# Performance work log

Hardware: AMD Instinct MI355X
Metric: run time of the kernel (lower is better)

## Reference

```python
import jax, jax.numpy as jnp
import numpy as np

EPS = 1e-5
H = 12  # num_heads

def ste_sign(x):
    # forward: sign(x) in {-1,+1}; backward: grad passes where |x|<1 (clip STE)
    c = jnp.clip(x, -1.0, 1.0)
    s = jnp.where(x >= 0, 1.0, -1.0).astype(x.dtype)
    return c + jax.lax.stop_gradient(s - c)

def bin_w(w):
    # adaptive per-output-channel scaling: alpha = mean|w| (detached), weight = alpha*sign(w)
    alpha = jax.lax.stop_gradient(jnp.mean(jnp.abs(w), axis=1, keepdims=True))
    return alpha * ste_sign(w)

def layernorm(x, g, b):
    mu = jnp.mean(x, axis=-1, keepdims=True)
    var = jnp.var(x, axis=-1, keepdims=True)
    return (x - mu) * jax.lax.rsqrt(var + EPS) * g + b

def setup_inputs():
    key = jax.random.key(0)
    ks = jax.random.split(key, 6)
    B, N, C, hid = 8, 1024, 768, 3072
    s = 0.02
    return {
        "x": jax.random.normal(ks[0], (B, N, C), jnp.float32),
        "ln1_g": jnp.ones((C,), jnp.float32),
        "ln1_b": jnp.zeros((C,), jnp.float32),
        "w_qkv": jax.random.normal(ks[1], (3 * C, C), jnp.float32) * s,
        "w_proj": jax.random.normal(ks[2], (C, C), jnp.float32) * s,
        "b_proj": jnp.zeros((C,), jnp.float32),
        "ls1_g": 1e-5 * jnp.ones((C,), jnp.float32),
        "ln2_g": jnp.ones((C,), jnp.float32),
        "ln2_b": jnp.zeros((C,), jnp.float32),
        "w_fc1": jax.random.normal(ks[3], (hid, C), jnp.float32) * s,
        "b_fc1": jnp.zeros((hid,), jnp.float32),
        "w_fc2": jax.random.normal(ks[4], (C, hid), jnp.float32) * s,
        "b_fc2": jnp.zeros((C,), jnp.float32),
        "ls2_g": 1e-5 * jnp.ones((C,), jnp.float32),
    }

def reference(x, ln1_g, ln1_b, w_qkv, w_proj, b_proj, ls1_g, ln2_g, ln2_b, w_fc1, b_fc1, w_fc2, b_fc2, ls2_g):
    B, N, C = x.shape
    hd = C // H
    scale = hd ** -0.5
    # --- binarized attention ---
    h = layernorm(x, ln1_g, ln1_b)
    qkv = jnp.einsum('bnc,oc->bno', ste_sign(h), bin_w(w_qkv))        # 1w1a qkv proj
    qkv = qkv.reshape(B, N, 3, H, hd).transpose(2, 0, 3, 1, 4)        # [3,B,H,N,hd]
    bqkv = ste_sign(qkv)                                              # BinaryQuantizer
    q, k, v = bqkv[0], bqkv[1], bqkv[2]
    attn = jnp.einsum('bhnd,bhmd->bhnm', q, k) * scale                # [B,H,N,N]
    sm = jax.nn.softmax(attn, axis=-1)
    abin = (attn > 0).astype(x.dtype)                                 # SoftmaxBinaryQuantizer fwd value
    attn_eff = sm + jax.lax.stop_gradient(abin - sm)                  # STE: fwd=binary, bwd=softmax
    o = jnp.einsum('bhnm,bhmd->bhnd', attn_eff, v)
    o = o.transpose(0, 2, 1, 3).reshape(B, N, C)
    o = jnp.einsum('bnc,oc->bno', ste_sign(o), bin_w(w_proj)) + b_proj
    x = x + ls1_g * o
    # --- binary MLP (1-bit weight, 32-bit activation) ---
    h2 = layernorm(x, ln2_g, ln2_b)
    m = jax.nn.gelu(jnp.einsum('bnc,hc->bnh', h2, bin_w(w_fc1)) + b_fc1, approximate=False)
    m = jnp.einsum('bnh,ch->bnc', m, bin_w(w_fc2)) + b_fc2
    return x + ls2_g * m
```

## Files before the change

### kernel.cpp

```cpp
#include <hip/hip_runtime.h>

#define NTOK 8192
#define CDIM 768
#define HIDD 3072
#define NQKV 2304
#define SEQL 1024
#define NHEAD 12

typedef int i32x4 __attribute__((ext_vector_type(4)));
typedef float f32x4 __attribute__((ext_vector_type(4)));
typedef signed char sc16 __attribute__((ext_vector_type(16)));

__device__ __forceinline__ void gload_lds16(const void* g, void* l) {
    __builtin_amdgcn_global_load_lds(
        (const __attribute__((address_space(1))) unsigned int*)g,
        (__attribute__((address_space(3))) unsigned int*)l, 16, 0, 0);
}

__global__ void sign_w_kernel(const float* __restrict__ w, signed char* __restrict__ ws, int n) {
    int i = blockIdx.x * blockDim.x + threadIdx.x;
    int stride = gridDim.x * blockDim.x;
    for (; i < n; i += stride)
        ws[i] = (w[i] >= 0.0f) ? 1 : -1;
}

template<bool PERM>
__global__ void __launch_bounds__(256) signalpha_kernel(const float* __restrict__ w,
                                                        signed char* __restrict__ ws,
                                                        float* __restrict__ alpha, int K) {
    int row = blockIdx.x;
    const float* wr = w + (size_t)row * K;
    signed char* wsr = ws + (size_t)row * K;
    float s = 0.f;
    for (int i = threadIdx.x; i < K; i += 256) {
        float v = wr[i];
        int ip = PERM ? ((i & ~63) | (((i & 15) << 2) | ((i >> 4) & 3))) : i;
        wsr[ip] = (v >= 0.f) ? 1 : -1;
        s += fabsf(v);
    }
    for (int off = 32; off > 0; off >>= 1) s += __shfl_down(s, off);
    __shared__ float red[4];
    if ((threadIdx.x & 63) == 0) red[threadIdx.x >> 6] = s;
    __syncthreads();
    if (threadIdx.x == 0) alpha[row] = (red[0] + red[1] + red[2] + red[3]) / (float)K;
}

__global__ void __launch_bounds__(256) ln_sign_kernel(const float* __restrict__ x, const float* __restrict__ g,
                                                      const float* __restrict__ b, signed char* __restrict__ out) {
    int row = blockIdx.x;
    const float* xr = x + (size_t)row * CDIM;
    float v0 = xr[threadIdx.x], v1 = xr[threadIdx.x + 256], v2 = xr[threadIdx.x + 512];
    float s = v0 + v1 + v2, s2 = v0 * v0 + v1 * v1 + v2 * v2;
    for (int off = 32; off > 0; off >>= 1) { s += __shfl_down(s, off); s2 += __shfl_down(s2, off); }
    __shared__ float red[8];
    if ((threadIdx.x & 63) == 0) { red[threadIdx.x >> 6] = s; red[4 + (threadIdx.x >> 6)] = s2; }
    __syncthreads();
    float ts = red[0] + red[1] + red[2] + red[3];
    float t2 = red[4] + red[5] + red[6] + red[7];
    float mu = ts * (1.0f / CDIM);
    float var = t2 * (1.0f / CDIM) - mu * mu;
    float rstd = rsqrtf(var + 1e-5f);
    signed char* orow = out + (size_t)row * CDIM;
    float vv[3] = {v0, v1, v2};
#pragma unroll
    for (int p = 0; p < 3; p++) {
        int i = threadIdx.x + p * 256;
        float val = (vv[p] - mu) * rstd * g[i] + b[i];
        orow[i] = (val >= 0.f) ? 1 : -1;
    }
}

__global__ void __launch_bounds__(256) ln2q_kernel(const float* __restrict__ x, const float* __restrict__ g,
                                                   const float* __restrict__ b, signed char* __restrict__ out,
                                                   float* __restrict__ rowscale) {
    int row = blockIdx.x;
    const float* xr = x + (size_t)row * CDIM;
    float v0 = xr[threadIdx.x], v1 = xr[threadIdx.x + 256], v2 = xr[threadIdx.x + 512];
    float s = v0 + v1 + v2, s2 = v0 * v0 + v1 * v1 + v2 * v2;
    for (int off = 32; off > 0; off >>= 1) { s += __shfl_down(s, off); s2 += __shfl_down(s2, off); }
    __shared__ float red[8];
    __shared__ float redm[4];
    if ((threadIdx.x & 63) == 0) { red[threadIdx.x >> 6] = s; red[4 + (threadIdx.x >> 6)] = s2; }
    __syncthreads();
    float ts = red[0] + red[1] + red[2] + red[3];
    float t2 = red[4] + red[5] + red[6] + red[7];
    float mu = ts * (1.0f / CDIM);
    float var = t2 * (1.0f / CDIM) - mu * mu;
    float rstd = rsqrtf(var + 1e-5f);
    float a0 = (v0 - mu) * rstd * g[threadIdx.x] + b[threadIdx.x];
    float a1 = (v1 - mu) * rstd * g[threadIdx.x + 256] + b[threadIdx.x + 256];
    float a2v = (v2 - mu) * rstd * g[threadIdx.x + 512] + b[threadIdx.x + 512];
    float mx = fmaxf(fabsf(a0), fmaxf(fabsf(a1), fabsf(a2v)));
    for (int off = 32; off > 0; off >>= 1) mx = fmaxf(mx, __shfl_down(mx, off));
    if ((threadIdx.x & 63) == 0) redm[threadIdx.x >> 6] = mx;
    __syncthreads();
    float rmax = fmaxf(fmaxf(redm[0], redm[1]), fmaxf(redm[2], redm[3]));
    rmax = fmaxf(rmax, 1e-20f);
    float inv = 127.f / rmax;
    signed char* orow = out + (size_t)row * CDIM;
    orow[threadIdx.x]       = (signed char)__float2int_rn(a0 * inv);
    orow[threadIdx.x + 256] = (signed char)__float2int_rn(a1 * inv);
    orow[threadIdx.x + 512] = (signed char)__float2int_rn(a2v * inv);
    if (threadIdx.x == 0) rowscale[row] = rmax * (1.f / 127.f);
}

enum { EPI_RESID = 1, EPI_GELU = 2, EPI_QKV = 3 };
#define MSCALE_INV 16.0f

template<int EPI, int BN>
__global__ void __launch_bounds__(256) gemm_i8(
    const signed char* __restrict__ A, const signed char* __restrict__ B,
    int M, int N, int K,
    const float* __restrict__ alpha, const float* __restrict__ bias,
    const float* __restrict__ ls, const float* __restrict__ resid,
    const float* __restrict__ rowscale, float ascale,
    float* __restrict__ outF, signed char* __restrict__ outB,
    signed char* __restrict__ vtB)
{
    constexpr int STAGE_B = 3 * (128 + BN) * 64;
    static_assert(STAGE_B >= 128 * 68 * 4 || EPI != EPI_RESID, "epi lds fits");
    __shared__ __align__(16) char lds_raw[STAGE_B];
    auto As = (signed char (*)[128][64])lds_raw;
    auto Bs = (signed char (*)[BN][64])(lds_raw + 3 * 128 * 64);

    const int tid = threadIdx.x, ln = tid & 63, w = tid >> 6;
    const int wm = w >> 1, wn = w & 1;
    const int lq = ln & 15, khi = ln >> 4;
    constexpr int NF = BN / 32;
    constexpr int L = (BN == 128) ? 4 : 3;

    const int nwg = gridDim.x * gridDim.y;
    const int id = blockIdx.y * gridDim.x + blockIdx.x;
    const int nid = (id & 7) * (nwg >> 3) + (id >> 3);
    const int bxs = nid % gridDim.x, bys = nid / gridDim.x;
    const int bm = bys * 128, bn = bxs * BN;

    const i32x4 iz = {0, 0, 0, 0};
    i32x4 acc[4][NF];
#pragma unroll
    for (int m = 0; m < 4; m++)
#pragma unroll
        for (int n = 0; n < NF; n++) acc[m][n] = iz;

    const int srow = tid >> 2, scol = (tid & 3) * 16;
    const int ssrc = ((tid & 3) ^ ((srow >> 1) & 3)) * 16;
    const int sa = 16 * (khi ^ ((lq >> 1) & 3));

    auto STAGE = [&](int p, int k0) {
        gload_lds16(A + (size_t)(bm + srow) * K + k0 + ssrc, &As[p][srow][scol]);
        gload_lds16(A + (size_t)(bm + 64 + srow) * K + k0 + ssrc, &As[p][64 + srow][scol]);
        gload_lds16(B + (size_t)(bn + srow) * K + k0 + ssrc, &Bs[p][srow][scol]);
        if constexpr (BN == 128)
            gload_lds16(B + (size_t)(bn + 64 + srow) * K + k0 + ssrc, &Bs[p][64 + srow][scol]);
    };
    auto COMPUTE = [&](int p, bool prefetch, int knext) {
        i32x4 aF[4], bF[NF];
#pragma unroll
        for (int m = 0; m < 4; m++) aF[m] = *(const i32x4*)&As[p][wm * 64 + m * 16 + lq][sa];
#pragma unroll
        for (int n = 0; n < NF; n++) bF[n] = *(const i32x4*)&Bs[p][wn * (BN / 2) + n * 16 + lq][sa];
        if (prefetch) STAGE((p + 2) % 3, knext);
        __builtin_amdgcn_s_setprio(1);
#pragma unroll
        for (int m = 0; m < 4; m++)
#pragma unroll
            for (int n = 0; n < NF; n++)
                acc[m][n] = __builtin_amdgcn_mfma_i32_16x16x64_i8(aF[m], bF[n], acc[m][n], 0, 0, 0);
        __builtin_amdgcn_s_setprio(0);
    };

    const int nst = K >> 6;
    STAGE(0, 0);
    STAGE(1, 64);
#pragma unroll 1
    for (int t = 0; t < nst - 1; t++) {
        asm volatile("s_waitcnt vmcnt(%0)" :: "n"(L) : "memory");
        __builtin_amdgcn_s_barrier();
        COMPUTE(t % 3, t + 2 < nst, (t + 2) << 6);
    }
    asm volatile("s_waitcnt vmcnt(0)" ::: "memory");
    __builtin_amdgcn_s_barrier();
    COMPUTE((nst - 1) % 3, false, 0);

    const int r0 = bm + wm * 64, c0loc = wn * (BN / 2);

    if constexpr (EPI == EPI_RESID) {
        __syncthreads();
        float (*Cf)[68] = (float (*)[68])lds_raw;
#pragma unroll
        for (int m = 0; m < 4; m++)
#pragma unroll
            for (int n = 0; n < NF; n++)
#pragma unroll
                for (int i = 0; i < 4; i++)
                    Cf[wm * 64 + m * 16 + khi * 4 + i][c0loc + n * 16 + lq] =
                        (float)acc[m][n][i] * ascale;
        __syncthreads();
#pragma unroll
        for (int p = 0; p < 8; p++) {
            int idx = p * 256 + tid;
            int row = idx >> 4, c4 = (idx & 15) * 4;
            f32x4 a4 = *(const f32x4*)&alpha[bn + c4];
            f32x4 b4 = *(const f32x4*)&bias[bn + c4];
            f32x4 l4 = *(const f32x4*)&ls[bn + c4];
            f32x4 v4 = *(const f32x4*)&Cf[row][c4];
            size_t g = (size_t)(bm + row) * N + bn + c4;
            f32x4 r4 = *(const f32x4*)&resid[g];
            f32x4 o4 = r4 + l4 * (a4 * v4 + b4);
            *(f32x4*)&outF[g] = o4;
        }
    } else if constexpr (EPI == EPI_GELU) {
        float al[NF], bi[NF];
#pragma unroll
        for (int n = 0; n < NF; n++) {
            int c = bn + c0loc + n * 16 + lq;
            al[n] = alpha[c]; bi[n] = bias[c];
        }
#pragma unroll
        for (int m = 0; m < 4; m++)
#pragma unroll
            for (int i = 0; i < 4; i++) {
                int r = r0 + m * 16 + khi * 4 + i;
                float rs = rowscale[r];
                unsigned pk = 0;
#pragma unroll
                for (int n = 0; n < NF; n++) {
                    float t = al[n] * ((float)acc[m][n][i] * rs) + bi[n];
                    float y2 = 1.5957691f * t + 0.07135481f * t * t * t;
                    float ge = t * __builtin_amdgcn_rcpf(1.0f + __expf(-y2));
                    float qf = fminf(fmaxf(ge * MSCALE_INV, -127.f), 127.f);
                    pk |= (unsigned)(unsigned char)(signed char)__float2int_rn(qf) << (8 * n);
                }
                *(unsigned*)(outB + (size_t)r * N + bn + c0loc + lq * 4) = pk;
            }
    } else {
        if (bn < 1536) {
#pragma unroll
            for (int m = 0; m < 4; m++)
#pragma unroll
                for (int i = 0; i < 4; i++) {
                    int r = r0 + m * 16 + khi * 4 + i;
                    unsigned pk = 0;
#pragma unroll
                    for (int n = 0; n < NF; n++)
                        pk |= (unsigned)(unsigned char)(signed char)((acc[m][n][i] >= 0) ? 1 : -1) << (8 * n);
                    *(unsigned*)(outB + (size_t)r * 1536 + bn + c0loc + lq * 4) = pk;
                }
        } else {
#pragma unroll
            for (int m = 0; m < 4; m++)
#pragma unroll
                for (int n = 0; n < NF; n++) {
                    int cg = bn + c0loc + n * 16 + lq - 1536;
                    int hh = cg >> 6, dd = cg & 63;
                    int rb = r0 + m * 16 + khi * 4;
                    unsigned pk = 0;
#pragma unroll
                    for (int i = 0; i < 4; i++)
                        pk |= (unsigned)(unsigned char)(signed char)((acc[m][n][i] >= 0) ? 1 : -1) << (8 * i);
                    *(unsigned*)(vtB + (((size_t)(rb >> 10) * NHEAD + hh) * 64 + dd) * SEQL + (rb & 1023)) = pk;
                }
        }
    }
}

__global__ void __launch_bounds__(256) attn_v2(const signed char* __restrict__ qk,
                                               const signed char* __restrict__ vt,
                                               signed char* __restrict__ a2) {
    const int id = blockIdx.x;
    const int nid = (id & 7) * 96 + (id >> 3);
    const int bh = nid >> 3, qb = nid & 7;
    const int b = bh / NHEAD, h = bh % NHEAD;
    const int tid = threadIdx.x, ln = tid & 63, w = tid >> 6;
    const int lq = ln & 15, khi = ln >> 4;

    __shared__ signed char Ks[64][80];
    __shared__ signed char Vts[64][80];
    __shared__ signed char Pw[4][32][80];

    const size_t tokbase = (size_t)b * SEQL;
    const int q0 = qb * 128 + w * 32;
    const int str = tid >> 2, stc = (tid & 3) * 16;
    const size_t vtrow = ((size_t)bh * 64 + str) * SEQL;

    i32x4 qfrag[2];
#pragma unroll
    for (int qf = 0; qf < 2; qf++)
        qfrag[qf] = *(const i32x4*)(qk + (tokbase + q0 + qf * 16 + lq) * 1536 + h * 64 + khi * 16);

    const i32x4 iz = {0, 0, 0, 0};
    i32x4 o[2][4];
#pragma unroll
    for (int qf = 0; qf < 2; qf++)
#pragma unroll
        for (int df = 0; df < 4; df++) o[qf][df] = iz;

    auto LOADJ = [&](int j, sc16& kr, sc16& vr) {
        kr = *(const sc16*)(qk + (tokbase + j * 64 + str) * 1536 + 768 + h * 64 + stc);
        vr = *(const sc16*)(vt + vtrow + j * 64 + stc);
    };
    auto STORE = [&](const sc16& kr, const sc16& vr) {
        *(sc16*)&Ks[str][stc] = kr;
        *(sc16*)&Vts[str][stc] = vr;
    };
    auto COMPUTE = [&]() {
        i32x4 kfrag[4];
#pragma unroll
        for (int kf = 0; kf < 4; kf++)
            kfrag[kf] = *(const i32x4*)&Ks[kf * 16 + lq][khi * 16];
#pragma unroll
        for (int kf = 0; kf < 4; kf++) {
#pragma unroll
            for (int qf = 0; qf < 2; qf++) {
                i32x4 st = __builtin_amdgcn_mfma_i32_16x16x64_i8(kfrag[kf], qfrag[qf], iz, 0, 0, 0);
                unsigned pb = (st[0] > 0 ? 1u : 0u) | (st[1] > 0 ? 0x100u : 0u) |
                              (st[2] > 0 ? 0x10000u : 0u) | (st[3] > 0 ? 0x1000000u : 0u);
                *(unsigned*)&Pw[w][qf * 16 + lq][kf * 16 + khi * 4] = pb;
            }
        }
        i32x4 pa[2];
#pragma unroll
        for (int qf = 0; qf < 2; qf++)
            pa[qf] = *(const i32x4*)&Pw[w][qf * 16 + lq][khi * 16];
#pragma unroll
        for (int df = 0; df < 4; df++) {
            i32x4 vfr = *(const i32x4*)&Vts[df * 16 + lq][khi * 16];
#pragma unroll
            for (int qf = 0; qf < 2; qf++)
                o[qf][df] = __builtin_amdgcn_mfma_i32_16x16x64_i8(pa[qf], vfr, o[qf][df], 0, 0, 0);
        }
    };

    sc16 ka, va, kb, vb;
    LOADJ(0, ka, va);
#pragma unroll 1
    for (int jj = 0; jj < 16; jj += 2) {
        __syncthreads();
        STORE(ka, va);
        __syncthreads();
        LOADJ(jj + 1, kb, vb);
        COMPUTE();
        __syncthreads();
        STORE(kb, vb);
        __syncthreads();
        if (jj + 2 < 16) LOADJ(jj + 2, ka, va);
        COMPUTE();
    }

#pragma unroll
    for (int qf = 0; qf < 2; qf++)
#pragma unroll
        for (int i = 0; i < 4; i++) {
            int qrow = q0 + qf * 16 + khi * 4 + i;
            unsigned pk = 0;
#pragma unroll
            for (int df = 0; df < 4; df++)
                pk |= (unsigned)(unsigned char)(signed char)((o[qf][df][i] >= 0) ? 1 : -1) << (8 * df);
            *(unsigned*)(a2 + (tokbase + qrow) * CDIM + h * 64 + lq * 4) = pk;
        }
}

static const size_t OFF_WQKV  = 0;
static const size_t OFF_WPROJ = 1769472;
static const size_t OFF_WFC1  = 2359296;
static const size_t OFF_WFC2  = 4718592;
static const size_t OFF_APROJ = 7077888;
static const size_t OFF_AFC1  = 7080960;
static const size_t OFF_AFC2  = 7093248;
static const size_t OFF_H2SC  = 7096320;
static const size_t OFF_QK    = 7129088;
static const size_t OFF_VT    = 19712000;
static const size_t OFF_A2    = 26003456;
static const size_t OFF_A1    = 32294912;
static const size_t OFF_M1    = 38586368;
static const size_t OFF_H2    = 63752192;

extern "C" void kernel_launch(void* const* d_in, const int* in_sizes, int n_in,
                              void* d_out, int out_size, void* d_ws, size_t ws_size,
                              hipStream_t stream) {
    const float* x      = (const float*)d_in[0];
    const float* ln1_g  = (const float*)d_in[1];
    const float* ln1_b  = (const float*)d_in[2];
    const float* w_qkv  = (const float*)d_in[3];
    const float* w_proj = (const float*)d_in[4];
    const float* b_proj = (const float*)d_in[5];
    const float* ls1_g  = (const float*)d_in[6];
    const float* ln2_g  = (const float*)d_in[7];
    const float* ln2_b  = (const float*)d_in[8];
    const float* w_fc1  = (const float*)d_in[9];
    const float* b_fc1  = (const float*)d_in[10];
    const float* w_fc2  = (const float*)d_in[11];
    const float* b_fc2  = (const float*)d_in[12];
    const float* ls2_g  = (const float*)d_in[13];
    float* out = (float*)d_out;

    char* ws = (char*)d_ws;
    signed char* wqkv_s  = (signed char*)(ws + OFF_WQKV);
    signed char* wproj_s = (signed char*)(ws + OFF_WPROJ);
    signed char* wfc1_s  = (signed char*)(ws + OFF_WFC1);
    signed char* wfc2_s  = (signed char*)(ws + OFF_WFC2);
    float* a_proj  = (float*)(ws + OFF_APROJ);
    float* a_fc1   = (float*)(ws + OFF_AFC1);
    float* a_fc2   = (float*)(ws + OFF_AFC2);
    float* h2scale = (float*)(ws + OFF_H2SC);
    signed char* qk   = (signed char*)(ws + OFF_QK);
    signed char* vt   = (signed char*)(ws + OFF_VT);
    signed char* a2   = (signed char*)(ws + OFF_A2);
    signed char* a1   = (signed char*)(ws + OFF_A1);
    signed char* m1   = (signed char*)(ws + OFF_M1);
    signed char* h2   = (signed char*)(ws + OFF_H2);

    sign_w_kernel<<<512, 256, 0, stream>>>(w_qkv, wqkv_s, NQKV * CDIM);
    signalpha_kernel<true><<<CDIM, 256, 0, stream>>>(w_proj, wproj_s, a_proj, CDIM);
    signalpha_kernel<false><<<HIDD, 256, 0, stream>>>(w_fc1,  wfc1_s,  a_fc1,  CDIM);
    signalpha_kernel<true><<<CDIM, 256, 0, stream>>>(w_fc2,  wfc2_s,  a_fc2,  HIDD);

    ln_sign_kernel<<<NTOK, 256, 0, stream>>>(x, ln1_g, ln1_b, a1);

    gemm_i8<EPI_QKV, 128><<<dim3(NQKV / 128, NTOK / 128), 256, 0, stream>>>(
        a1, wqkv_s, NTOK, NQKV, CDIM, nullptr, nullptr, nullptr, nullptr, nullptr, 1.0f, nullptr, qk, vt);

    attn_v2<<<768, 256, 0, stream>>>(qk, vt, a2);

    gemm_i8<EPI_RESID, 64><<<dim3(CDIM / 64, NTOK / 128), 256, 0, stream>>>(
        a2, wproj_s, NTOK, CDIM, CDIM, a_proj, b_proj, ls1_g, x, nullptr, 1.0f, out, nullptr, nullptr);

    ln2q_kernel<<<NTOK, 256, 0, stream>>>(out, ln2_g, ln2_b, h2, h2scale);

    gemm_i8<EPI_GELU, 128><<<dim3(HIDD / 128, NTOK / 128), 256, 0, stream>>>(
        h2, wfc1_s, NTOK, HIDD, CDIM, a_fc1, b_fc1, nullptr, nullptr, h2scale, 1.0f, nullptr, m1, nullptr);

    gemm_i8<EPI_RESID, 64><<<dim3(CDIM / 64, NTOK / 128), 256, 0, stream>>>(
        m1, wfc2_s, NTOK, CDIM, HIDD, a_fc2, b_fc2, ls2_g, out, nullptr, 1.0f / MSCALE_INV, out, nullptr, nullptr);
}
```

Baseline: 170.9 us.

## Use dedicated 64x64-tile GEMM with residual prefetch for proj and fc2

Replaces the 128x64-tile residual-epilogue instantiation with a separate 64x64-tile kernel for the proj and fc2 GEMMs. The grid doubles from 768 to 1536 workgroups, which improves occupancy and wave balance on N=768 outputs. The residual, alpha, bias and layer-scale values are now loaded before the K loop, so their latency overlaps the main loop. Each workgroup computes less per loaded operand tile, so A/B reuse drops, and more registers are held across the loop for the prefetched residual.

```diff
diff --git a/kernel.cpp b/kernel.cpp
--- a/kernel.cpp
+++ b/kernel.cpp
@@ -104,7 +104,7 @@
     if (threadIdx.x == 0) rowscale[row] = rmax * (1.f / 127.f);
 }
 
-enum { EPI_RESID = 1, EPI_GELU = 2, EPI_QKV = 3 };
+enum { EPI_GELU = 2, EPI_QKV = 3 };
 #define MSCALE_INV 16.0f
 
 template<int EPI, int BN>
@@ -112,14 +112,10 @@
     const signed char* __restrict__ A, const signed char* __restrict__ B,
     int M, int N, int K,
     const float* __restrict__ alpha, const float* __restrict__ bias,
-    const float* __restrict__ ls, const float* __restrict__ resid,
-    const float* __restrict__ rowscale, float ascale,
-    float* __restrict__ outF, signed char* __restrict__ outB,
-    signed char* __restrict__ vtB)
+    const float* __restrict__ rowscale,
+    signed char* __restrict__ outB, signed char* __restrict__ vtB)
 {
-    constexpr int STAGE_B = 3 * (128 + BN) * 64;
-    static_assert(STAGE_B >= 128 * 68 * 4 || EPI != EPI_RESID, "epi lds fits");
-    __shared__ __align__(16) char lds_raw[STAGE_B];
+    __shared__ __align__(16) char lds_raw[3 * (128 + BN) * 64];
     auto As = (signed char (*)[128][64])lds_raw;
     auto Bs = (signed char (*)[BN][64])(lds_raw + 3 * 128 * 64);
 
@@ -184,32 +180,7 @@
 
     const int r0 = bm + wm * 64, c0loc = wn * (BN / 2);
 
-    if constexpr (EPI == EPI_RESID) {
-        __syncthreads();
-        float (*Cf)[68] = (float (*)[68])lds_raw;
-#pragma unroll
-        for (int m = 0; m < 4; m++)
-#pragma unroll
-            for (int n = 0; n < NF; n++)
-#pragma unroll
-                for (int i = 0; i < 4; i++)
-                    Cf[wm * 64 + m * 16 + khi * 4 + i][c0loc + n * 16 + lq] =
-                        (float)acc[m][n][i] * ascale;
-        __syncthreads();
-#pragma unroll
-        for (int p = 0; p < 8; p++) {
-            int idx = p * 256 + tid;
-            int row = idx >> 4, c4 = (idx & 15) * 4;
-            f32x4 a4 = *(const f32x4*)&alpha[bn + c4];
-            f32x4 b4 = *(const f32x4*)&bias[bn + c4];
-            f32x4 l4 = *(const f32x4*)&ls[bn + c4];
-            f32x4 v4 = *(const f32x4*)&Cf[row][c4];
-            size_t g = (size_t)(bm + row) * N + bn + c4;
-            f32x4 r4 = *(const f32x4*)&resid[g];
-            f32x4 o4 = r4 + l4 * (a4 * v4 + b4);
-            *(f32x4*)&outF[g] = o4;
-        }
-    } else if constexpr (EPI == EPI_GELU) {
+    if constexpr (EPI == EPI_GELU) {
         float al[NF], bi[NF];
 #pragma unroll
         for (int n = 0; n < NF; n++) {
@@ -261,6 +232,95 @@
                     *(unsigned*)(vtB + (((size_t)(rb >> 10) * NHEAD + hh) * 64 + dd) * SEQL + (rb & 1023)) = pk;
                 }
         }
+    }
+}
+
+__global__ void __launch_bounds__(256) gemm_resid(
+    const signed char* __restrict__ A, const signed char* __restrict__ B,
+    int N, int K,
+    const float* __restrict__ alpha, const float* __restrict__ bias,
+    const float* __restrict__ ls, const float* __restrict__ resid,
+    float ascale, float* __restrict__ outF)
+{
+    __shared__ __align__(16) char lds_raw[24576];
+    auto As = (signed char (*)[64][64])lds_raw;
+    auto Bs = (signed char (*)[64][64])(lds_raw + 3 * 64 * 64);
+
+    const int tid = threadIdx.x, ln = tid & 63, w = tid >> 6;
+    const int wm = w >> 1, wn = w & 1;
+    const int lq = ln & 15, khi = ln >> 4;
+
+    const int nwg = gridDim.x * gridDim.y;
+    const int id = blockIdx.y * gridDim.x + blockIdx.x;
+    const int nid = (id & 7) * (nwg >> 3) + (id >> 3);
+    const int bxs = nid % gridDim.x, bys = nid / gridDim.x;
+    const int bm = bys * 64, bn = bxs * 64;
+
+    const int ec4 = (tid & 15) * 4, erow0 = tid >> 4;
+    f32x4 a4 = *(const f32x4*)&alpha[bn + ec4];
+    f32x4 b4 = *(const f32x4*)&bias[bn + ec4];
+    f32x4 l4 = *(const f32x4*)&ls[bn + ec4];
+    f32x4 r4[4];
+#pragma unroll
+    for (int p = 0; p < 4; p++)
+        r4[p] = *(const f32x4*)&resid[(size_t)(bm + erow0 + p * 16) * N + bn + ec4];
+
+    const i32x4 iz = {0, 0, 0, 0};
+    i32x4 acc[2][2] = {{iz, iz}, {iz, iz}};
+
+    const int srow = tid >> 2, scol = (tid & 3) * 16;
+    const int ssrc = ((tid & 3) ^ ((srow >> 1) & 3)) * 16;
+    const int sa = 16 * (khi ^ ((lq >> 1) & 3));
+
+    auto STAGE = [&](int p, int k0) {
+        gload_lds16(A + (size_t)(bm + srow) * K + k0 + ssrc, &As[p][srow][scol]);
+        gload_lds16(B + (size_t)(bn + srow) * K + k0 + ssrc, &Bs[p][srow][scol]);
+    };
+    auto COMPUTE = [&](int p, bool prefetch, int knext) {
+        i32x4 aF[2], bF[2];
+#pragma unroll
+        for (int m = 0; m < 2; m++) aF[m] = *(const i32x4*)&As[p][wm * 32 + m * 16 + lq][sa];
+#pragma unroll
+        for (int n = 0; n < 2; n++) bF[n] = *(const i32x4*)&Bs[p][wn * 32 + n * 16 + lq][sa];
+        if (prefetch) STAGE((p + 2) % 3, knext);
+        __builtin_amdgcn_s_setprio(1);
+#pragma unroll
+        for (int m = 0; m < 2; m++)
+#pragma unroll
+            for (int n = 0; n < 2; n++)
+                acc[m][n] = __builtin_amdgcn_mfma_i32_16x16x64_i8(aF[m], bF[n], acc[m][n], 0, 0, 0);
+        __builtin_amdgcn_s_setprio(0);
+    };
+
+    const int nst = K >> 6;
+    STAGE(0, 0);
+    STAGE(1, 64);
+#pragma unroll 1
+    for (int t = 0; t < nst - 1; t++) {
+        asm volatile("s_waitcnt vmcnt(2)" ::: "memory");
+        __builtin_amdgcn_s_barrier();
+        COMPUTE(t % 3, t + 2 < nst, (t + 2) << 6);
+    }
+    asm volatile("s_waitcnt vmcnt(0)" ::: "memory");
+    __builtin_amdgcn_s_barrier();
+    COMPUTE((nst - 1) % 3, false, 0);
+
+    __syncthreads();
+    float (*Cf)[68] = (float (*)[68])lds_raw;
+#pragma unroll
+    for (int m = 0; m < 2; m++)
+#pragma unroll
+        for (int n = 0; n < 2; n++)
+#pragma unroll
+            for (int i = 0; i < 4; i++)
+                Cf[wm * 32 + m * 16 + khi * 4 + i][wn * 32 + n * 16 + lq] =
+                    (float)acc[m][n][i] * ascale;
+    __syncthreads();
+#pragma unroll
+    for (int p = 0; p < 4; p++) {
+        f32x4 v4 = *(const f32x4*)&Cf[erow0 + p * 16][ec4];
+        f32x4 o4 = r4[p] + l4 * (a4 * v4 + b4);
+        *(f32x4*)&outF[(size_t)(bm + erow0 + p * 16) * N + bn + ec4] = o4;
     }
 }
 
@@ -418,18 +478,18 @@
     ln_sign_kernel<<<NTOK, 256, 0, stream>>>(x, ln1_g, ln1_b, a1);
 
     gemm_i8<EPI_QKV, 128><<<dim3(NQKV / 128, NTOK / 128), 256, 0, stream>>>(
-        a1, wqkv_s, NTOK, NQKV, CDIM, nullptr, nullptr, nullptr, nullptr, nullptr, 1.0f, nullptr, qk, vt);
+        a1, wqkv_s, NTOK, NQKV, CDIM, nullptr, nullptr, nullptr, qk, vt);
 
     attn_v2<<<768, 256, 0, stream>>>(qk, vt, a2);
 
-    gemm_i8<EPI_RESID, 64><<<dim3(CDIM / 64, NTOK / 128), 256, 0, stream>>>(
-        a2, wproj_s, NTOK, CDIM, CDIM, a_proj, b_proj, ls1_g, x, nullptr, 1.0f, out, nullptr, nullptr);
+    gemm_resid<<<dim3(CDIM / 64, NTOK / 64), 256, 0, stream>>>(
+        a2, wproj_s, CDIM, CDIM, a_proj, b_proj, ls1_g, x, 1.0f, out);
 
     ln2q_kernel<<<NTOK, 256, 0, stream>>>(out, ln2_g, ln2_b, h2, h2scale);
 
     gemm_i8<EPI_GELU, 128><<<dim3(HIDD / 128, NTOK / 128), 256, 0, stream>>>(
-        h2, wfc1_s, NTOK, HIDD, CDIM, a_fc1, b_fc1, nullptr, nullptr, h2scale, 1.0f, nullptr, m1, nullptr);
-
-    gemm_i8<EPI_RESID, 64><<<dim3(CDIM / 64, NTOK / 128), 256, 0, stream>>>(
-        m1, wfc2_s, NTOK, CDIM, HIDD, a_fc2, b_fc2, ls2_g, out, nullptr, 1.0f / MSCALE_INV, out, nullptr, nullptr);
-}
+        h2, wfc1_s, NTOK, HIDD, CDIM, a_fc1, b_fc1, h2scale, m1, nullptr);
+
+    gemm_resid<<<dim3(CDIM / 64, NTOK / 64), 256, 0, stream>>>(
+        m1, wfc2_s, CDIM, HIDD, a_fc2, b_fc2, ls2_g, out, 1.0f / MSCALE_INV, out);
+}
```

New measurement: 181.9 us. 1.06x slower.

## Use 256x128 eight-wave int8 GEMM tiles and bf16 intermediate residual

Applied to the files above, without the earlier changes.

Replaces the 128xBN three-stage int8 GEMM with a 256x128 tile run by 512 threads (8 waves), using a double-buffered LDS pipeline split into k-subtiles with staggered prefetch. The residual-epilogue GEMMs now prefetch residual and scale vectors before the main loop. The post-attention hidden state is stored as bf16 in a reused workspace region, which halves traffic for the LN2 read and the FC2 residual read. The bf16 rounding of the residual adds precision loss, and the larger tiles cut the number of workgroups for the N=768 GEMMs.

```diff
diff --git a/kernel.cpp b/kernel.cpp
--- a/kernel.cpp
+++ b/kernel.cpp
@@ -10,6 +10,16 @@
 typedef int i32x4 __attribute__((ext_vector_type(4)));
 typedef float f32x4 __attribute__((ext_vector_type(4)));
 typedef signed char sc16 __attribute__((ext_vector_type(16)));
+typedef unsigned short us4 __attribute__((ext_vector_type(4)));
+
+__device__ __forceinline__ unsigned short f32_to_bf16(float f) {
+    unsigned int u = __float_as_uint(f);
+    u += 0x7FFFu + ((u >> 16) & 1u);
+    return (unsigned short)(u >> 16);
+}
+__device__ __forceinline__ float bf16_to_f32(unsigned short h) {
+    return __uint_as_float(((unsigned)h) << 16);
+}
 
 __device__ __forceinline__ void gload_lds16(const void* g, void* l) {
     __builtin_amdgcn_global_load_lds(
@@ -70,12 +80,14 @@
     }
 }
 
-__global__ void __launch_bounds__(256) ln2q_kernel(const float* __restrict__ x, const float* __restrict__ g,
+__global__ void __launch_bounds__(256) ln2q_kernel(const unsigned short* __restrict__ x, const float* __restrict__ g,
                                                    const float* __restrict__ b, signed char* __restrict__ out,
                                                    float* __restrict__ rowscale) {
     int row = blockIdx.x;
-    const float* xr = x + (size_t)row * CDIM;
-    float v0 = xr[threadIdx.x], v1 = xr[threadIdx.x + 256], v2 = xr[threadIdx.x + 512];
+    const unsigned short* xr = x + (size_t)row * CDIM;
+    float v0 = bf16_to_f32(xr[threadIdx.x]);
+    float v1 = bf16_to_f32(xr[threadIdx.x + 256]);
+    float v2 = bf16_to_f32(xr[threadIdx.x + 512]);
     float s = v0 + v1 + v2, s2 = v0 * v0 + v1 * v1 + v2 * v2;
     for (int off = 32; off > 0; off >>= 1) { s += __shfl_down(s, off); s2 += __shfl_down(s2, off); }
     __shared__ float red[8];
@@ -104,162 +116,209 @@
     if (threadIdx.x == 0) rowscale[row] = rmax * (1.f / 127.f);
 }
 
-enum { EPI_RESID = 1, EPI_GELU = 2, EPI_QKV = 3 };
+enum { EPI_QKV = 0, EPI_GELU = 1, EPI_PROJ = 2, EPI_FC2 = 3 };
 #define MSCALE_INV 16.0f
 
-template<int EPI, int BN>
-__global__ void __launch_bounds__(256) gemm_i8(
+template<int EPI>
+__global__ void __launch_bounds__(512, 2) gemm8p(
     const signed char* __restrict__ A, const signed char* __restrict__ B,
-    int M, int N, int K,
+    int N, int K,
     const float* __restrict__ alpha, const float* __restrict__ bias,
-    const float* __restrict__ ls, const float* __restrict__ resid,
+    const float* __restrict__ ls,
+    const float* __restrict__ residF, const unsigned short* __restrict__ residH,
     const float* __restrict__ rowscale, float ascale,
-    float* __restrict__ outF, signed char* __restrict__ outB,
-    signed char* __restrict__ vtB)
+    float* __restrict__ outF, unsigned short* __restrict__ outH,
+    signed char* __restrict__ outB, signed char* __restrict__ vtB)
 {
-    constexpr int STAGE_B = 3 * (128 + BN) * 64;
-    static_assert(STAGE_B >= 128 * 68 * 4 || EPI != EPI_RESID, "epi lds fits");
-    __shared__ __align__(16) char lds_raw[STAGE_B];
-    auto As = (signed char (*)[128][64])lds_raw;
-    auto Bs = (signed char (*)[BN][64])(lds_raw + 3 * 128 * 64);
+    __shared__ __align__(16) char lds_raw[98304];
+    auto Ab = (signed char (*)[2][256][64])lds_raw;
+    auto Bb = (signed char (*)[2][128][64])(lds_raw + 65536);
 
     const int tid = threadIdx.x, ln = tid & 63, w = tid >> 6;
-    const int wm = w >> 1, wn = w & 1;
+    const int wm = w >> 2, wn = w & 3;
     const int lq = ln & 15, khi = ln >> 4;
-    constexpr int NF = BN / 32;
-    constexpr int L = (BN == 128) ? 4 : 3;
 
     const int nwg = gridDim.x * gridDim.y;
     const int id = blockIdx.y * gridDim.x + blockIdx.x;
     const int nid = (id & 7) * (nwg >> 3) + (id >> 3);
     const int bxs = nid % gridDim.x, bys = nid / gridDim.x;
-    const int bm = bys * 128, bn = bxs * BN;
+    const int bm = bys * 256, bn = bxs * 128;
+
+    const int ec4 = (tid & 31) * 4, er = tid >> 5;
+    f32x4 a4, b4, l4;
+    f32x4 rF[16];
+    us4 rH[16];
+    if constexpr (EPI >= EPI_PROJ) {
+        a4 = *(const f32x4*)&alpha[bn + ec4];
+        b4 = *(const f32x4*)&bias[bn + ec4];
+        l4 = *(const f32x4*)&ls[bn + ec4];
+#pragma unroll
+        for (int h = 0; h < 2; h++)
+#pragma unroll
+            for (int q = 0; q < 8; q++) {
+                size_t g = (size_t)(bm + h * 128 + q * 16 + er) * N + bn + ec4;
+                if constexpr (EPI == EPI_FC2) rH[h * 8 + q] = *(const us4*)&residH[g];
+                else                          rF[h * 8 + q] = *(const f32x4*)&residF[g];
+            }
+    }
 
     const i32x4 iz = {0, 0, 0, 0};
-    i32x4 acc[4][NF];
-#pragma unroll
-    for (int m = 0; m < 4; m++)
-#pragma unroll
-        for (int n = 0; n < NF; n++) acc[m][n] = iz;
-
-    const int srow = tid >> 2, scol = (tid & 3) * 16;
-    const int ssrc = ((tid & 3) ^ ((srow >> 1) & 3)) * 16;
+    i32x4 acc[8][2];
+#pragma unroll
+    for (int m = 0; m < 8; m++)
+#pragma unroll
+        for (int n = 0; n < 2; n++) acc[m][n] = iz;
+
+    const int gsw = ((tid & 3) ^ ((tid >> 3) & 3)) * 16;
     const int sa = 16 * (khi ^ ((lq >> 1) & 3));
-
-    auto STAGE = [&](int p, int k0) {
-        gload_lds16(A + (size_t)(bm + srow) * K + k0 + ssrc, &As[p][srow][scol]);
-        gload_lds16(A + (size_t)(bm + 64 + srow) * K + k0 + ssrc, &As[p][64 + srow][scol]);
-        gload_lds16(B + (size_t)(bn + srow) * K + k0 + ssrc, &Bs[p][srow][scol]);
-        if constexpr (BN == 128)
-            gload_lds16(B + (size_t)(bn + 64 + srow) * K + k0 + ssrc, &Bs[p][64 + srow][scol]);
+    const int sr4 = tid >> 2, sc = (tid & 3) * 16;
+
+    auto STAGE_A = [&](int d, int kt, int ks) {
+#pragma unroll
+        for (int j = 0; j < 2; j++) {
+            int row = j * 128 + sr4;
+            gload_lds16(A + (size_t)(bm + row) * K + kt * 128 + ks * 64 + gsw,
+                        &Ab[d][ks][row][sc]);
+        }
     };
-    auto COMPUTE = [&](int p, bool prefetch, int knext) {
-        i32x4 aF[4], bF[NF];
-#pragma unroll
-        for (int m = 0; m < 4; m++) aF[m] = *(const i32x4*)&As[p][wm * 64 + m * 16 + lq][sa];
-#pragma unroll
-        for (int n = 0; n < NF; n++) bF[n] = *(const i32x4*)&Bs[p][wn * (BN / 2) + n * 16 + lq][sa];
-        if (prefetch) STAGE((p + 2) % 3, knext);
-        __builtin_amdgcn_s_setprio(1);
-#pragma unroll
-        for (int m = 0; m < 4; m++)
-#pragma unroll
-            for (int n = 0; n < NF; n++)
-                acc[m][n] = __builtin_amdgcn_mfma_i32_16x16x64_i8(aF[m], bF[n], acc[m][n], 0, 0, 0);
-        __builtin_amdgcn_s_setprio(0);
+    auto STAGE_B = [&](int d, int kt, int ks) {
+        int row = sr4 & 127;
+        gload_lds16(B + (size_t)(bn + row) * K + kt * 128 + ks * 64 + gsw,
+                    &Bb[d][ks][row][sc]);
     };
 
-    const int nst = K >> 6;
-    STAGE(0, 0);
-    STAGE(1, 64);
+    const int nst = K >> 7;
+    STAGE_A(0, 0, 0); STAGE_B(0, 0, 0); STAGE_A(0, 0, 1); STAGE_B(0, 0, 1);
+    asm volatile("s_waitcnt vmcnt(3)" ::: "memory");
+    __builtin_amdgcn_s_barrier();
+
+    int cur = 0;
 #pragma unroll 1
-    for (int t = 0; t < nst - 1; t++) {
-        asm volatile("s_waitcnt vmcnt(%0)" :: "n"(L) : "memory");
-        __builtin_amdgcn_s_barrier();
-        COMPUTE(t % 3, t + 2 < nst, (t + 2) << 6);
+    for (int t = 0; t < nst; t++) {
+        const bool hn = (t + 1 < nst);
+#pragma unroll
+        for (int p = 0; p < 4; p++) {
+            const int ks = p >> 1, mq = p & 1;
+            i32x4 aF[4], bF[2];
+#pragma unroll
+            for (int mf = 0; mf < 4; mf++)
+                aF[mf] = *(const i32x4*)&Ab[cur][ks][wm * 128 + mq * 64 + mf * 16 + lq][sa];
+#pragma unroll
+            for (int nf = 0; nf < 2; nf++)
+                bF[nf] = *(const i32x4*)&Bb[cur][ks][wn * 32 + nf * 16 + lq][sa];
+            if (hn) {
+                if (p == 0)      STAGE_A(cur ^ 1, t + 1, 0);
+                else if (p == 1) STAGE_B(cur ^ 1, t + 1, 0);
+                else if (p == 2) STAGE_A(cur ^ 1, t + 1, 1);
+                else             STAGE_B(cur ^ 1, t + 1, 1);
+            }
+            __builtin_amdgcn_s_barrier();
+            __builtin_amdgcn_s_setprio(1);
+#pragma unroll
+            for (int mf = 0; mf < 4; mf++)
+#pragma unroll
+                for (int nf = 0; nf < 2; nf++)
+                    acc[mq * 4 + mf][nf] =
+                        __builtin_amdgcn_mfma_i32_16x16x64_i8(aF[mf], bF[nf], acc[mq * 4 + mf][nf], 0, 0, 0);
+            __builtin_amdgcn_s_setprio(0);
+            if (p == 1 || p == 3) {
+                if (hn) asm volatile("s_waitcnt vmcnt(3)" ::: "memory");
+                else    asm volatile("s_waitcnt vmcnt(0)" ::: "memory");
+            }
+            __builtin_amdgcn_s_barrier();
+        }
+        cur ^= 1;
     }
-    asm volatile("s_waitcnt vmcnt(0)" ::: "memory");
-    __builtin_amdgcn_s_barrier();
-    COMPUTE((nst - 1) % 3, false, 0);
-
-    const int r0 = bm + wm * 64, c0loc = wn * (BN / 2);
-
-    if constexpr (EPI == EPI_RESID) {
-        __syncthreads();
-        float (*Cf)[68] = (float (*)[68])lds_raw;
-#pragma unroll
-        for (int m = 0; m < 4; m++)
-#pragma unroll
-            for (int n = 0; n < NF; n++)
-#pragma unroll
-                for (int i = 0; i < 4; i++)
-                    Cf[wm * 64 + m * 16 + khi * 4 + i][c0loc + n * 16 + lq] =
-                        (float)acc[m][n][i] * ascale;
-        __syncthreads();
-#pragma unroll
-        for (int p = 0; p < 8; p++) {
-            int idx = p * 256 + tid;
-            int row = idx >> 4, c4 = (idx & 15) * 4;
-            f32x4 a4 = *(const f32x4*)&alpha[bn + c4];
-            f32x4 b4 = *(const f32x4*)&bias[bn + c4];
-            f32x4 l4 = *(const f32x4*)&ls[bn + c4];
-            f32x4 v4 = *(const f32x4*)&Cf[row][c4];
-            size_t g = (size_t)(bm + row) * N + bn + c4;
-            f32x4 r4 = *(const f32x4*)&resid[g];
-            f32x4 o4 = r4 + l4 * (a4 * v4 + b4);
-            *(f32x4*)&outF[g] = o4;
+
+    const int r0 = bm + wm * 128;
+
+    if constexpr (EPI == EPI_QKV) {
+        if (bn < 1536) {
+#pragma unroll
+            for (int m = 0; m < 8; m++)
+#pragma unroll
+                for (int i = 0; i < 4; i++) {
+                    int r = r0 + m * 16 + khi * 4 + i;
+                    unsigned short pk =
+                        (unsigned short)(unsigned char)(signed char)((acc[m][0][i] >= 0) ? 1 : -1) |
+                        ((unsigned short)(unsigned char)(signed char)((acc[m][1][i] >= 0) ? 1 : -1) << 8);
+                    *(unsigned short*)(outB + (size_t)r * 1536 + bn + (wn >> 1) * 64 + lq * 4 + (wn & 1) * 2) = pk;
+                }
+        } else {
+#pragma unroll
+            for (int m = 0; m < 8; m++)
+#pragma unroll
+                for (int n = 0; n < 2; n++) {
+                    int cg = bn + wn * 32 + n * 16 + lq - 1536;
+                    int hh = cg >> 6, dd = cg & 63;
+                    int rb = r0 + m * 16 + khi * 4;
+                    unsigned pk = 0;
+#pragma unroll
+                    for (int i = 0; i < 4; i++)
+                        pk |= (unsigned)(unsigned char)(signed char)((acc[m][n][i] >= 0) ? 1 : -1) << (8 * i);
+                    *(unsigned*)(vtB + (((size_t)(rb >> 10) * NHEAD + hh) * 64 + dd) * SEQL + (rb & 1023)) = pk;
+                }
         }
     } else if constexpr (EPI == EPI_GELU) {
-        float al[NF], bi[NF];
-#pragma unroll
-        for (int n = 0; n < NF; n++) {
-            int c = bn + c0loc + n * 16 + lq;
+        float al[2], bi[2];
+#pragma unroll
+        for (int n = 0; n < 2; n++) {
+            int c = bn + wn * 32 + n * 16 + lq;
             al[n] = alpha[c]; bi[n] = bias[c];
         }
 #pragma unroll
-        for (int m = 0; m < 4; m++)
+        for (int m = 0; m < 8; m++)
 #pragma unroll
             for (int i = 0; i < 4; i++) {
                 int r = r0 + m * 16 + khi * 4 + i;
                 float rs = rowscale[r];
-                unsigned pk = 0;
-#pragma unroll
-                for (int n = 0; n < NF; n++) {
+                unsigned short pk = 0;
+#pragma unroll
+                for (int n = 0; n < 2; n++) {
                     float t = al[n] * ((float)acc[m][n][i] * rs) + bi[n];
                     float y2 = 1.5957691f * t + 0.07135481f * t * t * t;
                     float ge = t * __builtin_amdgcn_rcpf(1.0f + __expf(-y2));
                     float qf = fminf(fmaxf(ge * MSCALE_INV, -127.f), 127.f);
-                    pk |= (unsigned)(unsigned char)(signed char)__float2int_rn(qf) << (8 * n);
+                    pk |= (unsigned short)(unsigned char)(signed char)__float2int_rn(qf) << (8 * n);
                 }
-                *(unsigned*)(outB + (size_t)r * N + bn + c0loc + lq * 4) = pk;
+                *(unsigned short*)(outB + (size_t)r * N + bn + (wn >> 1) * 64 + lq * 4 + (wn & 1) * 2) = pk;
             }
     } else {
-        if (bn < 1536) {
-#pragma unroll
-            for (int m = 0; m < 4; m++)
-#pragma unroll
-                for (int i = 0; i < 4; i++) {
-                    int r = r0 + m * 16 + khi * 4 + i;
-                    unsigned pk = 0;
-#pragma unroll
-                    for (int n = 0; n < NF; n++)
-                        pk |= (unsigned)(unsigned char)(signed char)((acc[m][n][i] >= 0) ? 1 : -1) << (8 * n);
-                    *(unsigned*)(outB + (size_t)r * 1536 + bn + c0loc + lq * 4) = pk;
+        float (*Cf)[132] = (float (*)[132])lds_raw;
+#pragma unroll 1
+        for (int h = 0; h < 2; h++) {
+            __syncthreads();
+            if (wm == h) {
+#pragma unroll
+                for (int m = 0; m < 8; m++)
+#pragma unroll
+                    for (int n = 0; n < 2; n++)
+#pragma unroll
+                        for (int i = 0; i < 4; i++)
+                            Cf[m * 16 + khi * 4 + i][wn * 32 + n * 16 + lq] =
+                                (float)acc[m][n][i] * ascale;
+            }
+            __syncthreads();
+#pragma unroll
+            for (int q = 0; q < 8; q++) {
+                int row = q * 16 + er;
+                f32x4 v4 = *(const f32x4*)&Cf[row][ec4];
+                size_t g = (size_t)(bm + h * 128 + row) * N + bn + ec4;
+                if constexpr (EPI == EPI_FC2) {
+                    us4 rh = rH[h * 8 + q];
+                    f32x4 r;
+                    r.x = bf16_to_f32(rh.x); r.y = bf16_to_f32(rh.y);
+                    r.z = bf16_to_f32(rh.z); r.w = bf16_to_f32(rh.w);
+                    f32x4 o4 = r + l4 * (a4 * v4 + b4);
+                    *(f32x4*)&outF[g] = o4;
+                } else {
+                    f32x4 o4 = rF[h * 8 + q] + l4 * (a4 * v4 + b4);
+                    us4 hh;
+                    hh.x = f32_to_bf16(o4.x); hh.y = f32_to_bf16(o4.y);
+                    hh.z = f32_to_bf16(o4.z); hh.w = f32_to_bf16(o4.w);
+                    *(us4*)&outH[g] = hh;
                 }
-        } else {
-#pragma unroll
-            for (int m = 0; m < 4; m++)
-#pragma unroll
-                for (int n = 0; n < NF; n++) {
-                    int cg = bn + c0loc + n * 16 + lq - 1536;
-                    int hh = cg >> 6, dd = cg & 63;
-                    int rb = r0 + m * 16 + khi * 4;
-                    unsigned pk = 0;
-#pragma unroll
-                    for (int i = 0; i < 4; i++)
-                        pk |= (unsigned)(unsigned char)(signed char)((acc[m][n][i] >= 0) ? 1 : -1) << (8 * i);
-                    *(unsigned*)(vtB + (((size_t)(rb >> 10) * NHEAD + hh) * 64 + dd) * SEQL + (rb & 1023)) = pk;
-                }
+            }
         }
     }
 }
@@ -370,10 +429,11 @@
 static const size_t OFF_H2SC  = 7096320;
 static const size_t OFF_QK    = 7129088;
 static const size_t OFF_VT    = 19712000;
-static const size_t OFF_A2    = 26003456;
-static const size_t OFF_A1    = 32294912;
+static const size_t OFF_A1    = 26003456;
+static const size_t OFF_A2    = 32294912;
 static const size_t OFF_M1    = 38586368;
 static const size_t OFF_H2    = 63752192;
+static const size_t OFF_X1B   = OFF_QK;
 
 extern "C" void kernel_launch(void* const* d_in, const int* in_sizes, int n_in,
                               void* d_out, int out_size, void* d_ws, size_t ws_size,
@@ -405,10 +465,11 @@
     float* h2scale = (float*)(ws + OFF_H2SC);
     signed char* qk   = (signed char*)(ws + OFF_QK);
     signed char* vt   = (signed char*)(ws + OFF_VT);
+    signed char* a1   = (signed char*)(ws + OFF_A1);
     signed char* a2   = (signed char*)(ws + OFF_A2);
-    signed char* a1   = (signed char*)(ws + OFF_A1);
     signed char* m1   = (signed char*)(ws + OFF_M1);
     signed char* h2   = (signed char*)(ws + OFF_H2);
+    unsigned short* x1b = (unsigned short*)(ws + OFF_X1B);
 
     sign_w_kernel<<<512, 256, 0, stream>>>(w_qkv, wqkv_s, NQKV * CDIM);
     signalpha_kernel<true><<<CDIM, 256, 0, stream>>>(w_proj, wproj_s, a_proj, CDIM);
@@ -417,19 +478,23 @@
 
     ln_sign_kernel<<<NTOK, 256, 0, stream>>>(x, ln1_g, ln1_b, a1);
 
-    gemm_i8<EPI_QKV, 128><<<dim3(NQKV / 128, NTOK / 128), 256, 0, stream>>>(
-        a1, wqkv_s, NTOK, NQKV, CDIM, nullptr, nullptr, nullptr, nullptr, nullptr, 1.0f, nullptr, qk, vt);
+    gemm8p<EPI_QKV><<<dim3(NQKV / 128, NTOK / 256), 512, 0, stream>>>(
+        a1, wqkv_s, NQKV, CDIM, nullptr, nullptr, nullptr, nullptr, nullptr,
+        nullptr, 1.0f, nullptr, nullptr, qk, vt);
 
     attn_v2<<<768, 256, 0, stream>>>(qk, vt, a2);
 
-    gemm_i8<EPI_RESID, 64><<<dim3(CDIM / 64, NTOK / 128), 256, 0, stream>>>(
-        a2, wproj_s, NTOK, CDIM, CDIM, a_proj, b_proj, ls1_g, x, nullptr, 1.0f, out, nullptr, nullptr);
-
-    ln2q_kernel<<<NTOK, 256, 0, stream>>>(out, ln2_g, ln2_b, h2, h2scale);
-
-    gemm_i8<EPI_GELU, 128><<<dim3(HIDD / 128, NTOK / 128), 256, 0, stream>>>(
-        h2, wfc1_s, NTOK, HIDD, CDIM, a_fc1, b_fc1, nullptr, nullptr, h2scale, 1.0f, nullptr, m1, nullptr);
-
-    gemm_i8<EPI_RESID, 64><<<dim3(CDIM / 64, NTOK / 128), 256, 0, stream>>>(
-        m1, wfc2_s, NTOK, CDIM, HIDD, a_fc2, b_fc2, ls2_g, out, nullptr, 1.0f / MSCALE_INV, out, nullptr, nullptr);
-}
+    gemm8p<EPI_PROJ><<<dim3(CDIM / 128, NTOK / 256), 512, 0, stream>>>(
+        a2, wproj_s, CDIM, CDIM, a_proj, b_proj, ls1_g, x, nullptr,
+        nullptr, 1.0f, nullptr, x1b, nullptr, nullptr);
+
+    ln2q_kernel<<<NTOK, 256, 0, stream>>>(x1b, ln2_g, ln2_b, h2, h2scale);
+
+    gemm8p<EPI_GELU><<<dim3(HIDD / 128, NTOK / 256), 512, 0, stream>>>(
+        h2, wfc1_s, HIDD, CDIM, a_fc1, b_fc1, nullptr, nullptr, nullptr,
+        h2scale, 1.0f, nullptr, nullptr, m1, nullptr);
+
+    gemm8p<EPI_FC2><<<dim3(CDIM / 128, NTOK / 256), 512, 0, stream>>>(
+        m1, wfc2_s, CDIM, HIDD, a_fc2, b_fc2, ls2_g, nullptr, x1b,
+        nullptr, 1.0f / MSCALE_INV, out, nullptr, nullptr, nullptr);
+}
```

After: 251.4 us. 47.2% more time.
